# Performance work log

Measured on AMD Instinct MI355X. Metric: run time of the kernel, lower is better.

The kernel has to match this reference:

```python
import jax, jax.numpy as jnp
import numpy as np

B, L, D, DFF, MODES = 16, 1536, 512, 2048, 64
KERNELS = (3, 5, 7)


def setup_inputs() -> dict:
    key = jax.random.key(0)
    ks = jax.random.split(key, 12)
    scale = 1.0 / (D * D)
    f32 = jnp.float32
    return {
        "x": jax.random.normal(ks[0], (B, L, D), f32),
        "w_real": scale * jax.random.normal(ks[1], (D, D, MODES), f32),
        "w_imag": scale * jax.random.normal(ks[2], (D, D, MODES), f32),
        "conv1_w": jax.random.normal(ks[3], (DFF, D), f32) / np.sqrt(D).astype(np.float32),
        "conv2_w": jax.random.normal(ks[4], (D, DFF), f32) / np.sqrt(DFF).astype(np.float32),
        "d1_w1": jax.random.normal(ks[5], (D // 2, D), f32) / np.sqrt(D).astype(np.float32),
        "d1_b1": jnp.zeros((D // 2,), f32),
        "d1_w2": jax.random.normal(ks[6], (len(KERNELS), D // 2), f32) / np.sqrt(D // 2).astype(np.float32),
        "d1_b2": jnp.zeros((len(KERNELS),), f32),
        "d2_w1": jax.random.normal(ks[7], (D // 2, D), f32) / np.sqrt(D).astype(np.float32),
        "d2_b1": jnp.zeros((D // 2,), f32),
        "d2_w2": jax.random.normal(ks[8], (len(KERNELS), D // 2), f32) / np.sqrt(D // 2).astype(np.float32),
        "d2_b2": jnp.zeros((len(KERNELS),), f32),
    }


def _avg_pool1d(x, k):
    # torch AvgPool1d(kernel=k, stride=1, padding=k//2), count_include_pad=True:
    # zero-pad then divide by k everywhere. x: (B, L, D) -> (B, L, D) for odd k.
    pad = k // 2
    xp = jnp.pad(x, ((0, 0), (pad, pad), (0, 0)))
    cs = jnp.pad(jnp.cumsum(xp, axis=1), ((0, 0), (1, 0), (0, 0)))
    return (cs[:, k:, :] - cs[:, :-k, :]) / k


def _moe_decomp(x, w1, b1, w2, b2):
    # trends: (B, L, D, E)
    trends = jnp.stack([_avg_pool1d(x, k) for k in KERNELS], axis=-1)
    h = jax.nn.relu(jnp.einsum("bld,hd->blh", x, w1) + b1)
    logits = jnp.einsum("blh,eh->ble", h, w2) + b2
    gates = jax.nn.softmax(logits, axis=-1)[:, :, None, :]  # (B, L, 1, E)
    x_trend = jnp.sum(trends * gates, axis=-1)
    return x - x_trend  # seasonal component


def _fourier_block(x, w_real, w_imag):
    q_ft = jnp.fft.rfft(x, axis=1)  # (B, L//2+1, D) complex
    modes = min(MODES, q_ft.shape[1])
    weights = (w_real + 1j * w_imag).astype(jnp.complex64)  # (D, D, modes)
    # batched complex matmul over the kept modes (fuses the per-mode loop)
    out_m = jnp.einsum("bmd,dem->bme", q_ft[:, :modes, :], weights[:, :, :modes])
    out_ft = jnp.zeros((x.shape[0], x.shape[1] // 2 + 1, x.shape[2]), jnp.complex64)
    out_ft = out_ft.at[:, :modes, :].set(out_m)
    return jnp.fft.irfft(out_ft, n=x.shape[1], axis=1)


def reference(x, w_real, w_imag, conv1_w, conv2_w,
              d1_w1, d1_b1, d1_w2, d1_b2,
              d2_w1, d2_b1, d2_w2, d2_b2):
    # FEB-f + residual (dropout = identity in eval)
    x = x + _fourier_block(x, w_real, w_imag)
    x = _moe_decomp(x, d1_w1, d1_b1, d1_w2, d1_b2)
    # 1x1 conv FFN == per-token linear layers
    y = jax.nn.relu(jnp.einsum("bld,fd->blf", x, conv1_w))
    y = jnp.einsum("blf,df->bld", y, conv2_w)
    res = _moe_decomp(x + y, d2_w1, d2_b1, d2_w2, d2_b2)
    return res
```

## Files before the change

kernel.cpp:

```cpp
#include <hip/hip_runtime.h>

#define B_   16
#define L_   1536
#define D_   512
#define DFF_ 2048
#define NM   64
#define HID  256

typedef short short8  __attribute__((ext_vector_type(8)));
typedef short short4v __attribute__((ext_vector_type(4)));
typedef float f32x4   __attribute__((ext_vector_type(4)));

__device__ __forceinline__ float b2f(short s) {
  unsigned int u = ((unsigned int)(unsigned short)s) << 16;
  float f; __builtin_memcpy(&f, &u, 4); return f;
}
__device__ __forceinline__ short f2b(float f) {
  unsigned int u; __builtin_memcpy(&u, &f, 4);
  u += 0x7fffu + ((u >> 16) & 1u);
  return (short)(u >> 16);
}
__device__ __forceinline__ f32x4 zero4() {
  f32x4 v; v[0]=0.f; v[1]=0.f; v[2]=0.f; v[3]=0.f; return v;
}

#define MFMA(a,b,c) __builtin_amdgcn_mfma_f32_16x16x32_bf16((a),(b),(c),0,0,0)
#define SWZ(row, grp) (((row) << 6) + ((((grp) ^ ((row) & 7))) << 3))
#define GLDS16(gp, lp) __builtin_amdgcn_global_load_lds( \
    (const __attribute__((address_space(1))) void*)(gp), \
    (__attribute__((address_space(3))) void*)(lp), 16, 0, 0)

__global__ __launch_bounds__(256) void zero_out(float* __restrict__ o, int n) {
  int i = blockIdx.x * 256 + threadIdx.x;
  if (i < n) o[i] = 0.f;
}

__global__ __launch_bounds__(256) void prep_all(
    const float* __restrict__ conv1_w, const float* __restrict__ conv2_w,
    const float* __restrict__ d1_w1,  const float* __restrict__ d2_w1,
    short* __restrict__ c1, short* __restrict__ c2,
    short* __restrict__ dw1, short* __restrict__ dw2,
    short* __restrict__ tcs, short* __restrict__ basis)
{
  int blk = blockIdx.x;
  if (blk < 2304) {
    const float* s; short* d; int i;
    if (blk < 1024)      { s = conv1_w; d = c1;  i = blk * 256 + threadIdx.x; }
    else if (blk < 2048) { s = conv2_w; d = c2;  i = (blk - 1024) * 256 + threadIdx.x; }
    else if (blk < 2176) { s = d1_w1;   d = dw1; i = (blk - 2048) * 256 + threadIdx.x; }
    else                 { s = d2_w1;   d = dw2; i = (blk - 2176) * 256 + threadIdx.x; }
    f32x4 v = ((const f32x4*)s)[i];
    short4v o;
    #pragma unroll
    for (int j = 0; j < 4; ++j) o[j] = f2b(v[j]);
    ((short4v*)d)[i] = o;
    return;
  }
  if (blk < 3072) {
    int i = (blk - 2304) * 256 + threadIdx.x;
    int m = i / L_, l = i - m * L_;
    int mm = (m < 64) ? m : (m - 64);
    int r = (mm * l) % L_;
    float th = (float)r * (6.283185307179586f / (float)L_);
    float s, c; __sincosf(th, &s, &c);
    tcs[i] = f2b((m < 64) ? c : -s);
    return;
  }
  {
    int i = (blk - 3072) * 256 + threadIdx.x;
    int l = i >> 7, k = i & 127;
    int m = (k < 64) ? k : (k - 64);
    int r = (m * l) % L_;
    float th = (float)r * (6.283185307179586f / (float)L_);
    float s, c; __sincosf(th, &s, &c);
    float v = (k < 64) ? ((m == 0) ? 1.f : 2.f) * (1.f / (float)L_) * c
                       : (-2.f / (float)L_) * s;
    basis[i] = f2b(v);
  }
}

__global__ __launch_bounds__(256) void transpose_w(
    const float* __restrict__ wre, const float* __restrict__ wim,
    short* __restrict__ wtr, short* __restrict__ wti)
{
  __shared__ float tile[64][17];
  int dc = blockIdx.x, e = blockIdx.y, t = threadIdx.x;
  int zz = blockIdx.z;
  const float* w = (zz < 4) ? wre : wim;
  short* wt      = (zz < 4) ? wtr : wti;
  int mBase = (zz & 3) * 16;
  {
    int dl = t >> 2, mg = t & 3;
    f32x4 v = *(const f32x4*)(w + ((long)(dc * 64 + dl) * 512 + e) * 64 + mBase + mg * 4);
    tile[dl][mg*4+0] = v[0]; tile[dl][mg*4+1] = v[1];
    tile[dl][mg*4+2] = v[2]; tile[dl][mg*4+3] = v[3];
  }
  __syncthreads();
  if (t < 128) {
    int mr = t >> 3, dg = t & 7;
    short8 o;
    #pragma unroll
    for (int j = 0; j < 8; ++j) o[j] = f2b(tile[dg * 8 + j][mr]);
    *(short8*)(wt + ((long)(mBase + mr) * 512 + e) * 512 + dc * 64 + dg * 8) = o;
  }
}

__global__ __launch_bounds__(256) void transpose_x(const float* __restrict__ x,
                                                   short* __restrict__ xt) {
  __shared__ float tile[64][65];
  int dc = blockIdx.x, lc = blockIdx.y, b = blockIdx.z, t = threadIdx.x;
  const float* xb = x + (long)b * L_ * D_;
  #pragma unroll
  for (int i = 0; i < 4; ++i) {
    int idx = i * 256 + t; int ll = idx >> 4, dg = idx & 15;
    f32x4 v = *(const f32x4*)(xb + (long)(lc * 64 + ll) * D_ + dc * 64 + dg * 4);
    tile[ll][dg*4+0] = v[0]; tile[ll][dg*4+1] = v[1];
    tile[ll][dg*4+2] = v[2]; tile[ll][dg*4+3] = v[3];
  }
  __syncthreads();
  #pragma unroll
  for (int i = 0; i < 2; ++i) {
    int idx = i * 256 + t; int dl = idx >> 3, lg = idx & 7;
    short8 o;
    #pragma unroll
    for (int j = 0; j < 8; ++j) o[j] = f2b(tile[lg * 8 + j][dl]);
    *(short8*)(xt + ((long)b * D_ + dc * 64 + dl) * L_ + lc * 64 + lg * 8) = o;
  }
}

template<bool RELU, bool HASBIAS>
__global__ __launch_bounds__(256) void gemm64(
    const short* __restrict__ A, long ldA,
    const short* __restrict__ W, long ldW,
    const float* __restrict__ bias,
    short* __restrict__ outB, long csr, long csc, int K)
{
  __shared__ short lA[2][64 * 64];
  __shared__ short lW[2][64 * 64];
  const int t = threadIdx.x, lane = t & 63, wid = t >> 6;
  const int quad = lane >> 4, l15 = lane & 15;
  const int wm = (wid & 1) * 32, wn = (wid >> 1) * 32;
  const long row0 = (long)blockIdx.x * 64, col0 = (long)blockIdx.y * 64;
  const short* Ab = A + row0 * ldA;
  const short* Wb = W + col0 * ldW;

  int srcrow[2]; long srcoff[2];
  #pragma unroll
  for (int i = 0; i < 2; ++i) {
    int c = wid * 2 + i;
    int r = c * 8 + (lane >> 3);
    int g = (lane & 7) ^ (r & 7);
    srcrow[i] = r; srcoff[i] = g * 8;
  }

  f32x4 acc[2][2];
  #pragma unroll
  for (int i = 0; i < 2; ++i)
    #pragma unroll
    for (int j = 0; j < 2; ++j) acc[i][j] = zero4();

  const int nk = K >> 6;
  #pragma unroll
  for (int i = 0; i < 2; ++i) {
    int c = wid * 2 + i;
    GLDS16(Ab + (long)srcrow[i] * ldA + srcoff[i], lA[0] + c * 512);
    GLDS16(Wb + (long)srcrow[i] * ldW + srcoff[i], lW[0] + c * 512);
  }
  if (nk > 1) {
    #pragma unroll
    for (int i = 0; i < 2; ++i) {
      int c = wid * 2 + i;
      GLDS16(Ab + (long)srcrow[i] * ldA + 64 + srcoff[i], lA[1] + c * 512);
      GLDS16(Wb + (long)srcrow[i] * ldW + 64 + srcoff[i], lW[1] + c * 512);
    }
  }

  for (int it = 0; it < nk; ++it) {
    if (it + 1 < nk) asm volatile("s_waitcnt vmcnt(4)" ::: "memory");
    else             asm volatile("s_waitcnt vmcnt(0)" ::: "memory");
    __builtin_amdgcn_s_barrier();
    const int cur = it & 1;
    const short* bufA = lA[cur];
    const short* bufW = lW[cur];
    #pragma unroll
    for (int ks = 0; ks < 2; ++ks) {
      int gq = ks * 4 + quad;
      short8 a0 = *(const short8*)&bufA[SWZ(wm + l15, gq)];
      short8 a1 = *(const short8*)&bufA[SWZ(wm + 16 + l15, gq)];
      short8 b0 = *(const short8*)&bufW[SWZ(wn + l15, gq)];
      short8 b1 = *(const short8*)&bufW[SWZ(wn + 16 + l15, gq)];
      acc[0][0] = MFMA(a0, b0, acc[0][0]);
      acc[0][1] = MFMA(a0, b1, acc[0][1]);
      acc[1][0] = MFMA(a1, b0, acc[1][0]);
      acc[1][1] = MFMA(a1, b1, acc[1][1]);
    }
    asm volatile("s_waitcnt lgkmcnt(0)" ::: "memory");
    __builtin_amdgcn_s_barrier();
    const long kn = (long)(it + 2) * 64;
    if (kn < K) {
      #pragma unroll
      for (int i = 0; i < 2; ++i) {
        int c = wid * 2 + i;
        GLDS16(Ab + (long)srcrow[i] * ldA + kn + srcoff[i], lA[cur] + c * 512);
        GLDS16(Wb + (long)srcrow[i] * ldW + kn + srcoff[i], lW[cur] + c * 512);
      }
    }
  }

  #pragma unroll
  for (int ni = 0; ni < 2; ++ni) {
    long col = col0 + wn + ni * 16 + l15;
    float bvv = HASBIAS ? bias[col] : 0.f;
    #pragma unroll
    for (int mi = 0; mi < 2; ++mi) {
      #pragma unroll
      for (int r = 0; r < 4; ++r) {
        long row = row0 + wm + mi * 16 + quad * 4 + r;
        float v = acc[mi][ni][r];
        if (HASBIAS) v += bvv;
        if (RELU)    v = fmaxf(v, 0.f);
        outB[row * csr + col * csc] = f2b(v);
      }
    }
  }
}

template<bool RELU, bool HASBIAS, bool HASRES, bool RESB>
__global__ __launch_bounds__(256) void gemm128(
    const short* __restrict__ A, long ldA, long Az,
    const short* __restrict__ W, long ldW, long Wz,
    const float* __restrict__ bias,
    const void* __restrict__ res, long ldres, long resZ,
    short* __restrict__ outB, long ldC, long Cz, int K)
{
  __shared__ short lA[2][128 * 64];
  __shared__ short lW[2][128 * 64];
  const int t = threadIdx.x, lane = t & 63, wid = t >> 6;
  const int quad = lane >> 4, l15 = lane & 15;
  const int wm = (wid & 1) * 64, wn = (wid >> 1) * 64;
  const long row0 = (long)blockIdx.x * 128, col0 = (long)blockIdx.y * 128;
  const int z = blockIdx.z;
  const short* Ab = A + (long)z * Az + row0 * ldA;
  const short* Wb = W + (long)z * Wz + col0 * ldW;

  int srcrow[4]; long srcoff[4];
  #pragma unroll
  for (int i = 0; i < 4; ++i) {
    int c = wid * 4 + i;
    int r = c * 8 + (lane >> 3);
    int g = (lane & 7) ^ (r & 7);
    srcrow[i] = r; srcoff[i] = g * 8;
  }

  f32x4 acc[4][4];
  #pragma unroll
  for (int i = 0; i < 4; ++i)
    #pragma unroll
    for (int j = 0; j < 4; ++j) acc[i][j] = zero4();

  const int nk = K >> 6;
  #pragma unroll
  for (int i = 0; i < 4; ++i) {
    int c = wid * 4 + i;
    GLDS16(Ab + (long)srcrow[i] * ldA + srcoff[i], lA[0] + c * 512);
    GLDS16(Wb + (long)srcrow[i] * ldW + srcoff[i], lW[0] + c * 512);
  }
  if (nk > 1) {
    #pragma unroll
    for (int i = 0; i < 4; ++i) {
      int c = wid * 4 + i;
      GLDS16(Ab + (long)srcrow[i] * ldA + 64 + srcoff[i], lA[1] + c * 512);
      GLDS16(Wb + (long)srcrow[i] * ldW + 64 + srcoff[i], lW[1] + c * 512);
    }
  }

  for (int it = 0; it < nk; ++it) {
    if (it + 1 < nk) asm volatile("s_waitcnt vmcnt(8)" ::: "memory");
    else             asm volatile("s_waitcnt vmcnt(0)" ::: "memory");
    __builtin_amdgcn_s_barrier();
    const int cur = it & 1;
    const short* bufA = lA[cur];
    const short* bufW = lW[cur];
    #pragma unroll
    for (int ks = 0; ks < 2; ++ks) {
      int gq = ks * 4 + quad;
      short8 av[4], bv[4];
      #pragma unroll
      for (int mi = 0; mi < 4; ++mi) av[mi] = *(const short8*)&bufA[SWZ(wm + mi * 16 + l15, gq)];
      #pragma unroll
      for (int ni = 0; ni < 4; ++ni) bv[ni] = *(const short8*)&bufW[SWZ(wn + ni * 16 + l15, gq)];
      #pragma unroll
      for (int mi = 0; mi < 4; ++mi)
        #pragma unroll
        for (int ni = 0; ni < 4; ++ni)
          acc[mi][ni] = MFMA(av[mi], bv[ni], acc[mi][ni]);
    }
    asm volatile("s_waitcnt lgkmcnt(0)" ::: "memory");
    __builtin_amdgcn_s_barrier();
    const long kn = (long)(it + 2) * 64;
    if (kn < K) {
      #pragma unroll
      for (int i = 0; i < 4; ++i) {
        int c = wid * 4 + i;
        GLDS16(Ab + (long)srcrow[i] * ldA + kn + srcoff[i], lA[cur] + c * 512);
        GLDS16(Wb + (long)srcrow[i] * ldW + kn + srcoff[i], lW[cur] + c * 512);
      }
    }
  }

  #pragma unroll
  for (int ni = 0; ni < 4; ++ni) {
    long col = col0 + wn + ni * 16 + l15;
    float bvv = HASBIAS ? bias[col] : 0.f;
    #pragma unroll
    for (int mi = 0; mi < 4; ++mi) {
      #pragma unroll
      for (int r = 0; r < 4; ++r) {
        long row = row0 + wm + mi * 16 + quad * 4 + r;
        float v = acc[mi][ni][r];
        if (HASBIAS) v += bvv;
        if (RELU)    v = fmaxf(v, 0.f);
        if (HASRES) {
          long ro = (long)z * resZ + row * ldres + col;
          v += RESB ? b2f(((const short*)res)[ro]) : ((const float*)res)[ro];
        }
        outB[(long)z * Cz + row * ldC + col] = f2b(v);
      }
    }
  }
}

__global__ __launch_bounds__(256) void mode_gemm(
    const short* __restrict__ qr, const short* __restrict__ qi,
    const short* __restrict__ wr, const short* __restrict__ wi,
    short* __restrict__ outm)
{
  __shared__ short lqr[16 * 64], lqi[16 * 64], lwr[64 * 64], lwi[64 * 64];
  const int m = blockIdx.x, en = blockIdx.y;
  const int t = threadIdx.x, lane = t & 63, wid = t >> 6;
  const int quad = lane >> 4, l15 = lane & 15;
  const short* qrb = qr + (long)m * (B_ * D_);
  const short* qib = qi + (long)m * (B_ * D_);
  const short* wrb = wr + (long)m * (D_ * D_) + (long)en * 64 * D_;
  const short* wib = wi + (long)m * (D_ * D_) + (long)en * 64 * D_;
  f32x4 accr = zero4(), acci = zero4();
  for (int k0 = 0; k0 < D_; k0 += 64) {
    __syncthreads();
    {
      int idx = t & 127; int r = idx >> 3, cg = idx & 7;
      const short* src = (t < 128 ? qrb : qib) + r * D_ + k0 + cg * 8;
      short* dst = (t < 128) ? lqr : lqi;
      *(short8*)&dst[SWZ(r, cg)] = *(const short8*)src;
    }
    #pragma unroll
    for (int i = 0; i < 4; ++i) {
      int idx = i * 256 + t;
      int which = idx >> 9, idx2 = idx & 511;
      int r = idx2 >> 3, cg = idx2 & 7;
      const short* src = (which ? wib : wrb) + r * D_ + k0 + cg * 8;
      short* dst = which ? lwi : lwr;
      *(short8*)&dst[SWZ(r, cg)] = *(const short8*)src;
    }
    __syncthreads();
    #pragma unroll
    for (int ks = 0; ks < 2; ++ks) {
      int gq = ks * 4 + quad;
      short8 ar = *(const short8*)&lqr[SWZ(l15, gq)];
      short8 ai = *(const short8*)&lqi[SWZ(l15, gq)];
      short8 br = *(const short8*)&lwr[SWZ(wid * 16 + l15, gq)];
      short8 bi = *(const short8*)&lwi[SWZ(wid * 16 + l15, gq)];
      short8 nai;
      #pragma unroll
      for (int j = 0; j < 8; ++j) nai[j] = (short)(ai[j] ^ (short)0x8000);
      accr = MFMA(ar, br, accr);
      accr = MFMA(nai, bi, accr);
      acci = MFMA(ar, bi, acci);
      acci = MFMA(ai, br, acci);
    }
  }
  #pragma unroll
  for (int r = 0; r < 4; ++r) {
    int bb = quad * 4 + r;
    long e = (long)en * 64 + wid * 16 + l15;
    long base = ((long)bb * D_ + e) * 128 + m;
    outm[base]      = f2b(accr[r]);
    outm[base + 64] = f2b(acci[r]);
  }
}

template<bool OUTF, bool WRITEB>
__global__ __launch_bounds__(512) void combine_kernel(
    const short* __restrict__ xin, const short* __restrict__ h,
    const float* __restrict__ w2, const float* __restrict__ b2,
    float* __restrict__ outf, short* __restrict__ outb)
{
  __shared__ float lG[64][4];
  int lc = blockIdx.x, b = blockIdx.y, t = threadIdx.x;
  int wid = t >> 6, lane = t & 63;
  int l0 = lc * 64;
  #pragma unroll
  for (int pi = 0; pi < 8; ++pi) {
    int pos = wid * 8 + pi;
    long row = (long)b * L_ + l0 + pos;
    short4v hh = *(const short4v*)(h + row * HID + lane * 4);
    float hv[4];
    #pragma unroll
    for (int j = 0; j < 4; ++j) hv[j] = b2f(hh[j]);
    float lg[3];
    #pragma unroll
    for (int e = 0; e < 3; ++e) {
      const float* wrow = w2 + e * HID + lane * 4;
      float p = hv[0] * wrow[0] + hv[1] * wrow[1] + hv[2] * wrow[2] + hv[3] * wrow[3];
      #pragma unroll
      for (int off = 32; off >= 1; off >>= 1) p += __shfl_xor(p, off);
      lg[e] = p + b2[e];
    }
    float mx = fmaxf(lg[0], fmaxf(lg[1], lg[2]));
    float e0 = __expf(lg[0] - mx), e1 = __expf(lg[1] - mx), e2 = __expf(lg[2] - mx);
    float inv = 1.f / (e0 + e1 + e2);
    float gv = (lane == 0) ? e0 * inv : (lane == 1) ? e1 * inv : e2 * inv;
    if (lane < 3) lG[pos][lane] = gv;
  }
  __syncthreads();

  int d = t;
  const short* xb = xin + (long)b * L_ * D_ + d;
  float win[7];
  #pragma unroll
  for (int j = 0; j < 6; ++j) {
    int l = l0 - 3 + j;
    win[j] = (l >= 0 && l < L_) ? b2f(xb[(long)l * D_]) : 0.f;
  }
  for (int i = 0; i < 64; ++i) {
    int lcn = l0 + i;
    int lr = lcn + 3;
    win[6] = (lr < L_) ? b2f(xb[(long)lr * D_]) : 0.f;
    float s3 = win[2] + win[3] + win[4];
    float s5 = s3 + win[1] + win[5];
    float s7 = s5 + win[0] + win[6];
    float trend = lG[i][0] * s3 * (1.f / 3.f) + lG[i][1] * s5 * (1.f / 5.f)
                + lG[i][2] * s7 * (1.f / 7.f);
    float v = win[3] - trend;
    long o = ((long)b * L_ + lcn) * D_ + d;
    if (OUTF)   outf[o] = v;
    if (WRITEB) outb[o] = f2b(v);
    #pragma unroll
    for (int j = 0; j < 6; ++j) win[j] = win[j + 1];
  }
}

extern "C" void kernel_launch(void* const* d_in, const int* in_sizes, int n_in,
                              void* d_out, int out_size, void* d_ws, size_t ws_size,
                              hipStream_t stream) {
  const float* x       = (const float*)d_in[0];
  const float* w_real  = (const float*)d_in[1];
  const float* w_imag  = (const float*)d_in[2];
  const float* conv1_w = (const float*)d_in[3];
  const float* conv2_w = (const float*)d_in[4];
  const float* d1_w1   = (const float*)d_in[5];
  const float* d1_b1   = (const float*)d_in[6];
  const float* d1_w2   = (const float*)d_in[7];
  const float* d1_b2   = (const float*)d_in[8];
  const float* d2_w1   = (const float*)d_in[9];
  const float* d2_b1   = (const float*)d_in[10];
  const float* d2_w2   = (const float*)d_in[11];
  const float* d2_b2   = (const float*)d_in[12];
  float* OUT = (float*)d_out;

  const size_t REQ_BIG = 144703488, REQ_SMALL = 98566144;
  if (ws_size < REQ_SMALL) {
    zero_out<<<(out_size + 255) / 256, 256, 0, stream>>>(OUT, out_size);
    return;
  }
  const bool big = (ws_size >= REQ_BIG);

  char* ws = (char*)d_ws;
  short* C1WB  = (short*)(ws + 0);
  short* C2WB  = (short*)(ws + 2097152);
  short* D1W1B = (short*)(ws + 4194304);
  short* D2W1B = (short*)(ws + 4456448);
  short* TCS   = (short*)(ws + 4718592);
  short* BASIS = (short*)(ws + 5111808);
  short* XT    = (short*)(ws + 6291456);
  short* Y1    = XT;
  short* QRI   = (short*)(ws + 31457280);
  short* OUTM  = (short*)(ws + 33554432);
  short* WTR   = (short*)(ws + 35651584);
  short* X1B   = WTR;
  short* WTI   = (short*)(ws + 69206016);
  short* X2B   = (short*)(ws + (big ? 106954752 : 60817408));
  short* H     = (short*)(ws + (big ? 132120576 : 85983232));

  prep_all<<<3840, 256, 0, stream>>>(conv1_w, conv2_w, d1_w1, d2_w1,
                                     C1WB, C2WB, D1W1B, D2W1B, TCS, BASIS);
  transpose_w<<<dim3(8, 512, 8), 256, 0, stream>>>(w_real, w_imag, WTR, WTI);
  transpose_x<<<dim3(8, 24, 16), 256, 0, stream>>>(x, XT);

  gemm64<false, false><<<dim3(128, 2), 256, 0, stream>>>(
      XT, L_, TCS, L_, nullptr, QRI, 1, (long)B_ * D_, L_);

  mode_gemm<<<dim3(64, 8), 256, 0, stream>>>(QRI, QRI + 64 * B_ * D_, WTR, WTI, OUTM);

  gemm128<false, false, true, false><<<dim3(12, 4, 16), 256, 0, stream>>>(
      BASIS, 128, 0, OUTM, 128, (long)D_ * 128, nullptr,
      x, D_, (long)L_ * D_, X1B, D_, (long)L_ * D_, 128);

  gemm64<true, true><<<dim3(384, 4), 256, 0, stream>>>(
      X1B, D_, D1W1B, D_, d1_b1, H, HID, 1, D_);
  combine_kernel<false, true><<<dim3(24, 16), 512, 0, stream>>>(
      X1B, H, d1_w2, d1_b2, nullptr, X2B);

  {
    const int nchunk = big ? 1 : 2;
    const long rows = big ? 24576 : 12288;
    for (int rc = 0; rc < nchunk; ++rc) {
      short* Ain = X2B + (long)rc * rows * D_;
      gemm128<true, false, false, false><<<dim3(rows / 128, 16, 1), 256, 0, stream>>>(
          Ain, D_, 0, C1WB, D_, 0, nullptr, nullptr, 0, 0, Y1, DFF_, 0, D_);
      gemm128<false, false, true, true><<<dim3(rows / 128, 4, 1), 256, 0, stream>>>(
          Y1, DFF_, 0, C2WB, DFF_, 0, nullptr, Ain, D_, 0, Ain, D_, 0, DFF_);
    }
  }

  gemm64<true, true><<<dim3(384, 4), 256, 0, stream>>>(
      X2B, D_, D2W1B, D_, d2_b1, H, HID, 1, D_);
  combine_kernel<true, false><<<dim3(24, 16), 512, 0, stream>>>(
      X2B, H, d2_w2, d2_b2, OUT, nullptr);
}
```

Before: 631.0 us.

## Add 256x256-tile double-buffered MFMA GEMM for the FFN layers

Replaces the two FFN GEMMs (conv1 with ReLU, conv2 with residual add) with a new 512-thread kernel using 256x256 output tiles, a two-stage LDS double buffer filled by global_load_lds, phased MFMA with barriers and setprio, and an XCD-aware block remap. The larger tile raises arithmetic intensity and cuts global re-reads of A and W, and the phase schedule is meant to overlap LDS reads, MFMAs and async loads. The cost is large register use (32 accumulators per lane), 128KB of LDS, and fewer workgroups, which may leave CUs idle or limit occupancy.

```diff
diff --git a/kernel.cpp b/kernel.cpp
--- a/kernel.cpp
+++ b/kernel.cpp
@@ -29,6 +29,7 @@
 #define GLDS16(gp, lp) __builtin_amdgcn_global_load_lds( \
     (const __attribute__((address_space(1))) void*)(gp), \
     (__attribute__((address_space(3))) void*)(lp), 16, 0, 0)
+#define MEMFENCE asm volatile("" ::: "memory")
 
 __global__ __launch_bounds__(256) void zero_out(float* __restrict__ o, int n) {
   int i = blockIdx.x * 256 + threadIdx.x;
@@ -328,6 +329,142 @@
       }
     }
   }
+}
+
+template<bool RELU, bool HASRES>
+__global__ __launch_bounds__(512, 2) void gemm256(
+    const short* __restrict__ A, long ldA,
+    const short* __restrict__ W, long ldW,
+    const short* __restrict__ res, long ldres,
+    short* __restrict__ outB, long ldC, int K, int gn)
+{
+  __shared__ short sh[65536];
+  const int t = threadIdx.x;
+  const int lane = t & 63, wid = t >> 6;
+  const int quad = lane >> 4, l15 = lane & 15;
+  const int wr = wid >> 2, wc = wid & 3;
+  const int wch = wc >> 1, cbw = (wc & 1) * 64;
+
+  const int nwg = gridDim.x;
+  const int cpx = nwg >> 3;
+  const int wg = (blockIdx.x & 7) * cpx + (blockIdx.x >> 3);
+  const int bx = wg / gn, by = wg - bx * gn;
+  const long row0 = (long)bx * 256, col0 = (long)by * 256;
+
+  const short* Ab = A + row0 * ldA;
+  const short* Wb = W + col0 * ldW;
+
+  const int srw = t >> 3;
+  const int sg  = (t & 7) ^ (srw & 7);
+
+#define STAGE(TP, KB) do {                                                   \
+    const long ko_ = (long)(KB) + sg * 8;                                    \
+    _Pragma("unroll")                                                        \
+    for (int h_ = 0; h_ < 2; ++h_) {                                         \
+      short* dA_ = sh + ((TP) * 2 + h_) * 8192;                              \
+      short* dB_ = sh + 32768 + ((TP) * 2 + h_) * 8192;                      \
+      _Pragma("unroll")                                                      \
+      for (int j_ = 0; j_ < 2; ++j_) {                                       \
+        const long gr_ = (long)(h_ * 128 + srw + j_ * 64);                   \
+        GLDS16(Ab + gr_ * ldA + ko_, dA_ + (j_ * 512 + t) * 8);              \
+        GLDS16(Wb + gr_ * ldW + ko_, dB_ + (j_ * 512 + t) * 8);              \
+      }                                                                      \
+    }                                                                        \
+  } while (0)
+
+  f32x4 acc[8][4];
+  #pragma unroll
+  for (int i = 0; i < 8; ++i)
+    #pragma unroll
+    for (int j = 0; j < 4; ++j) acc[i][j] = zero4();
+
+#define PH_LOADS(TP, QM, QN)                                                 \
+    const short* aS_ = sh + ((TP) * 2 + wr) * 8192;                          \
+    const short* bS_ = sh + 32768 + ((TP) * 2 + wch) * 8192;                 \
+    short8 av[4][2], bv[2][2];                                               \
+    _Pragma("unroll")                                                        \
+    for (int u = 0; u < 4; ++u)                                              \
+      _Pragma("unroll")                                                      \
+      for (int ks = 0; ks < 2; ++ks)                                         \
+        av[u][ks] = *(const short8*)&aS_[SWZ(((QM)*4+u)*16 + l15, ks*4 + quad)]; \
+    _Pragma("unroll")                                                        \
+    for (int v = 0; v < 2; ++v)                                              \
+      _Pragma("unroll")                                                      \
+      for (int ks = 0; ks < 2; ++ks)                                         \
+        bv[v][ks] = *(const short8*)&bS_[SWZ(cbw + ((QN)*2+v)*16 + l15, ks*4 + quad)];
+
+#define PH_MMA(QM, QN) do {                                                  \
+    asm volatile("s_waitcnt lgkmcnt(0)" ::: "memory");                       \
+    __builtin_amdgcn_s_setprio(1);                                           \
+    _Pragma("unroll")                                                        \
+    for (int ks = 0; ks < 2; ++ks)                                           \
+      _Pragma("unroll")                                                      \
+      for (int u = 0; u < 4; ++u)                                            \
+        _Pragma("unroll")                                                    \
+        for (int v = 0; v < 2; ++v)                                          \
+          acc[(QM)*4+u][(QN)*2+v] =                                          \
+              MFMA(av[u][ks], bv[v][ks], acc[(QM)*4+u][(QN)*2+v]);           \
+    __builtin_amdgcn_s_setprio(0);                                           \
+  } while (0)
+
+#define PH_LEAD(TP, QM, QN) do {                                             \
+    PH_LOADS(TP, QM, QN);                                                    \
+    PH_MMA(QM, QN);                                                          \
+    MEMFENCE; __builtin_amdgcn_s_barrier(); MEMFENCE;                        \
+  } while (0)
+
+#define PH_MID(TP, QM, QN) do {                                              \
+    PH_LOADS(TP, QM, QN);                                                    \
+    MEMFENCE; __builtin_amdgcn_s_barrier();                                  \
+    PH_MMA(QM, QN);                                                          \
+    MEMFENCE; __builtin_amdgcn_s_barrier(); MEMFENCE;                        \
+  } while (0)
+
+  const int NI = K >> 7;
+  STAGE(0, 0);
+
+  for (int i = 0; i < NI; ++i) {
+    const int kb = i << 7;
+    STAGE(1, kb + 64);
+    asm volatile("s_waitcnt vmcnt(8)" ::: "memory");
+    __builtin_amdgcn_s_barrier(); MEMFENCE;
+    PH_LEAD(0, 0, 0);
+    PH_MID(0, 1, 0);
+    PH_MID(0, 0, 1);
+    PH_MID(0, 1, 1);
+    if (i + 1 < NI) {
+      STAGE(0, kb + 128);
+      asm volatile("s_waitcnt vmcnt(8)" ::: "memory");
+    } else {
+      asm volatile("s_waitcnt vmcnt(0)" ::: "memory");
+    }
+    __builtin_amdgcn_s_barrier(); MEMFENCE;
+    PH_LEAD(1, 0, 0);
+    PH_MID(1, 1, 0);
+    PH_MID(1, 0, 1);
+    PH_MID(1, 1, 1);
+  }
+
+  #pragma unroll
+  for (int ni = 0; ni < 4; ++ni) {
+    long col = col0 + wc * 64 + ni * 16 + l15;
+    #pragma unroll
+    for (int mi = 0; mi < 8; ++mi) {
+      #pragma unroll
+      for (int r = 0; r < 4; ++r) {
+        long row = row0 + wr * 128 + mi * 16 + quad * 4 + r;
+        float v = acc[mi][ni][r];
+        if (RELU) v = fmaxf(v, 0.f);
+        if (HASRES) v += b2f(res[row * ldres + col]);
+        outB[row * ldC + col] = f2b(v);
+      }
+    }
+  }
+#undef STAGE
+#undef PH_LOADS
+#undef PH_MMA
+#undef PH_LEAD
+#undef PH_MID
 }
 
 __global__ __launch_bounds__(256) void mode_gemm(
@@ -513,12 +650,13 @@
   {
     const int nchunk = big ? 1 : 2;
     const long rows = big ? 24576 : 12288;
+    const int gm = (int)(rows / 256);
     for (int rc = 0; rc < nchunk; ++rc) {
       short* Ain = X2B + (long)rc * rows * D_;
-      gemm128<true, false, false, false><<<dim3(rows / 128, 16, 1), 256, 0, stream>>>(
-          Ain, D_, 0, C1WB, D_, 0, nullptr, nullptr, 0, 0, Y1, DFF_, 0, D_);
-      gemm128<false, false, true, true><<<dim3(rows / 128, 4, 1), 256, 0, stream>>>(
-          Y1, DFF_, 0, C2WB, DFF_, 0, nullptr, Ain, D_, 0, Ain, D_, 0, DFF_);
+      gemm256<true, false><<<dim3(gm * (DFF_ / 256)), 512, 0, stream>>>(
+          Ain, D_, C1WB, D_, nullptr, 0, Y1, DFF_, D_, DFF_ / 256);
+      gemm256<false, true><<<dim3(gm * (D_ / 256)), 512, 0, stream>>>(
+          Y1, DFF_, C2WB, DFF_, Ain, D_, Ain, D_, DFF_, D_ / 256);
     }
   }
 
```

New measurement: 586.5 us. -7.1%, faster.
